# Performance work log

Measured on AMD Instinct MI355X. Metric: run time of the kernel, lower is better.

## Reference

```python
import jax, jax.numpy as jnp
import numpy as np

EMBD = 768
FFN_HID = 2048
HEAD_DIM = 64
KV_H = 5
KV_DIM = KV_H * HEAD_DIM
Q_H = 15
EPS = 1.1920929e-07  # torch.finfo(float32).eps, nn.RMSNorm default when eps=None
MAX_WAVELENGTH = 10000.0


def rmsnorm(x, w):
    var = jnp.mean(x * x, axis=-1, keepdims=True)
    return x * jax.lax.rsqrt(var + EPS) * w


def apply_rope(q, L):
    # q: [B, L, H, D]; rotate-half RoPE applied only to queries (as in source)
    d_half = HEAD_DIM // 2
    ts = MAX_WAVELENGTH ** (2.0 / HEAD_DIM * jnp.arange(d_half, dtype=jnp.float32))
    pos = jnp.arange(L, dtype=jnp.float32)
    radians = pos[:, None] / ts[None, :]            # [L, d_half]
    s = jnp.sin(radians)[None, :, None, :]          # [1, L, 1, d_half]
    c = jnp.cos(radians)[None, :, None, :]
    q1, q2 = q[..., :d_half], q[..., d_half:]
    return jnp.concatenate([q1 * c - q2 * s, q2 * c + q1 * s], axis=-1)


def setup_inputs() -> dict:
    key = jax.random.key(0)
    ks = jax.random.split(key, 12)
    B, L, Lc = 4, 512, 2048
    sc = 0.02
    return {
        "x": jax.random.normal(ks[0], (B, L, EMBD), jnp.float32),
        "text_k": jax.random.normal(ks[1], (B, Lc, KV_DIM), jnp.float32),
        "text_v": jax.random.normal(ks[2], (B, Lc, KV_DIM), jnp.float32),
        "ln1_w": jnp.ones((EMBD,), jnp.float32),
        "ln2_w": jnp.ones((EMBD,), jnp.float32),
        "wq": jax.random.normal(ks[3], (EMBD, Q_H * HEAD_DIM), jnp.float32) * sc,
        "wk": jax.random.normal(ks[4], (KV_DIM, KV_DIM), jnp.float32) * sc,
        "wv": jax.random.normal(ks[5], (KV_DIM, KV_DIM), jnp.float32) * sc,
        "wo": jax.random.normal(ks[6], (Q_H * HEAD_DIM, EMBD), jnp.float32) * sc,
        "w_gate": jax.random.normal(ks[7], (EMBD, FFN_HID), jnp.float32) * sc,
        "w_up": jax.random.normal(ks[8], (EMBD, FFN_HID), jnp.float32) * sc,
        "w_down": jax.random.normal(ks[9], (FFN_HID, EMBD), jnp.float32) * sc,
    }


def reference(x, text_k, text_v, ln1_w, ln2_w, wq, wk, wv, wo, w_gate, w_up, w_down):
    B, L, _ = x.shape
    Lc = text_k.shape[1]

    residual = x
    x_norm = rmsnorm(x, ln1_w)
    q = (x_norm @ wq).reshape(B, L, Q_H, HEAD_DIM)
    k = (text_k @ wk).reshape(B, Lc, KV_H, HEAD_DIM)
    v = (text_v @ wv).reshape(B, Lc, KV_H, HEAD_DIM)

    q = apply_rope(q, L)

    # GQA: each of the 15 query heads maps to one of 5 kv heads
    kv_map = (jnp.arange(Q_H) * KV_H) // Q_H        # [0,0,0,1,1,1,...,4,4,4]
    k_sel = k[:, :, kv_map, :]                       # [B, Lc, Q_H, D]
    v_sel = v[:, :, kv_map, :]

    scores = jnp.einsum("blhd,bmhd->bhlm", q, k_sel) / (HEAD_DIM ** 0.5)
    attn = jax.nn.softmax(scores, axis=-1)
    ctx = jnp.einsum("bhlm,bmhd->blhd", attn, v_sel).reshape(B, L, Q_H * HEAD_DIM)

    x = ctx @ wo + residual

    residual = x
    xn = rmsnorm(x, ln2_w)
    h = jax.nn.silu(xn @ w_gate) * (xn @ w_up)       # SwiGLU
    return h @ w_down + residual
```

## Files before the change

### kernel.cpp

```cpp
#include <hip/hip_runtime.h>
#include <hip/hip_bf16.h>
#include <math.h>

#define EMBD 768
#define FFN_HID 2048
#define HEAD_DIM 64
#define KV_H 5
#define KV_DIM 320
#define Q_H 15
#define QDIM (Q_H * HEAD_DIM)
#define BB 4
#define LL 512
#define LC 2048
#define EPSV 1.1920929e-07f

typedef __attribute__((ext_vector_type(8))) __bf16 bf16x8;
typedef __attribute__((ext_vector_type(2))) __bf16 bf16x2;
typedef __attribute__((ext_vector_type(8))) short short8;
typedef __attribute__((ext_vector_type(4))) float floatx4;
typedef __attribute__((ext_vector_type(2))) unsigned uint2v;
typedef unsigned short ushort;

#define RSCALE 0.18033688011112042f

__device__ inline ushort f2bf(float f) {
  union { float f; unsigned u; } c; c.f = f;
  return (ushort)((c.u + 0x8000u) >> 16);
}
__device__ inline float bf2f(ushort s) {
  union { unsigned u; float f; } c; c.u = ((unsigned)s) << 16;
  return c.f;
}
#if __has_builtin(__builtin_amdgcn_cvt_pk_bf16_f32)
__device__ inline unsigned pk2bf(float a, float b) {
  union { bf16x2 v; unsigned u; } c;
  c.v = __builtin_amdgcn_cvt_pk_bf16_f32(a, b);
  return c.u;
}
#else
__device__ inline unsigned pk2bf(float a, float b) {
  union { float f; unsigned u; } x, y; x.f = a; y.f = b;
  return ((x.u + 0x8000u) >> 16) | ((y.u + 0x8000u) & 0xffff0000u);
}
#endif

__device__ __forceinline__ void glds16(const ushort* g, ushort* l) {
  __builtin_amdgcn_global_load_lds(
      (const __attribute__((address_space(1))) unsigned int*)g,
      (__attribute__((address_space(3))) unsigned int*)l, 16, 0, 0);
}

__global__ __launch_bounds__(256) void rmsnorm_kernel(const float* __restrict__ x,
                                                      const float* __restrict__ w,
                                                      ushort* __restrict__ out) {
  int row = blockIdx.x;
  const float* xr = x + (size_t)row * EMBD;
  ushort* orow = out + (size_t)row * EMBD;
  int tid = threadIdx.x;
  float ss = 0.f;
  for (int i = tid; i < EMBD; i += 256) { float v = xr[i]; ss += v * v; }
  for (int off = 32; off > 0; off >>= 1) ss += __shfl_down(ss, off, 64);
  __shared__ float sred[4];
  if ((tid & 63) == 0) sred[tid >> 6] = ss;
  __syncthreads();
  float tot = sred[0] + sred[1] + sred[2] + sred[3];
  float scale = rsqrtf(tot * (1.0f / EMBD) + EPSV);
  for (int i = tid; i < EMBD; i += 256) orow[i] = f2bf(xr[i] * scale * w[i]);
}

struct MD { const void* src; void* dst; const float* aux; int K; int N; int nx; int base; int mode; };
struct MD10 { MD d[10]; };

__global__ __launch_bounds__(256) void mega_prep(MD10 ds) {
  int bid = blockIdx.x;
  int sel = 0;
#pragma unroll
  for (int j = 1; j < 10; ++j) sel = (bid >= ds.d[j].base) ? j : sel;
  MD t = ds.d[sel];
  int rel = bid - t.base;
  int tid = threadIdx.x;
  if (t.mode == 1) {
    int i = rel * 256 + tid;
    float4 f = *(const float4*)((const float*)t.src + (size_t)i * 4);
    ushort* o = (ushort*)t.dst + (size_t)i * 4;
    o[0] = f2bf(f.x); o[1] = f2bf(f.y); o[2] = f2bf(f.z); o[3] = f2bf(f.w);
    return;
  }
  if (t.mode == 2) {
    const float* xr = (const float*)t.src + (size_t)rel * EMBD;
    ushort* orow = (ushort*)t.dst + (size_t)rel * EMBD;
    float ss = 0.f;
    for (int i = tid; i < EMBD; i += 256) { float v = xr[i]; ss += v * v; }
    for (int off = 32; off > 0; off >>= 1) ss += __shfl_down(ss, off, 64);
    __shared__ float sred[4];
    if ((tid & 63) == 0) sred[tid >> 6] = ss;
    __syncthreads();
    float tot = sred[0] + sred[1] + sred[2] + sred[3];
    float scale = rsqrtf(tot * (1.0f / EMBD) + EPSV);
    for (int i = tid; i < EMBD; i += 256) orow[i] = f2bf(xr[i] * scale * t.aux[i]);
    return;
  }
  int bx = rel % t.nx, by = rel / t.nx;
  int k0 = by * 64, n0 = bx * 64;
  __shared__ ushort T[64][72];
  int r = tid >> 2, cb = (tid & 3) * 16;
#pragma unroll
  for (int i = 0; i < 16; i += 4) {
    float4 f = *(const float4*)((const float*)t.src + (size_t)(k0 + r) * t.N + n0 + cb + i);
    T[r][cb + i + 0] = f2bf(f.x); T[r][cb + i + 1] = f2bf(f.y);
    T[r][cb + i + 2] = f2bf(f.z); T[r][cb + i + 3] = f2bf(f.w);
  }
  __syncthreads();
#pragma unroll
  for (int i = 0; i < 2; ++i) {
    short8 v;
#pragma unroll
    for (int j = 0; j < 8; ++j) v[j] = (short)T[cb + i * 8 + j][r];
    *(short8*)((ushort*)t.dst + (size_t)(n0 + r) * t.K + k0 + cb + i * 8) = v;
  }
}

template <int OM>
__global__ __launch_bounds__(256) void gemm64(const ushort* __restrict__ A,
                                              const ushort* __restrict__ Bt,
                                              const float* __restrict__ Rf,
                                              void* __restrict__ Cout,
                                              int M, int N, int K) {
  __shared__ ushort As[64 * 64];
  __shared__ ushort Bs[64 * 64];
  int tid = threadIdx.x;
  int w = tid >> 6, lane = tid & 63;
  int lm = lane & 15, lq = lane >> 4;
  int m0 = blockIdx.y * 64, n0 = blockIdx.x * 64;
  int wm = (w & 1) * 32, wn = (w >> 1) * 32;
  int arow = lane >> 3, acol = ((lane & 7) ^ arow) << 3;
  int kg[2] = {((lq) ^ (lm & 7)) << 3, ((4 + lq) ^ (lm & 7)) << 3};
  floatx4 acc[2][2];
#pragma unroll
  for (int i = 0; i < 2; ++i)
#pragma unroll
    for (int j = 0; j < 2; ++j) acc[i][j] = (floatx4){0.f, 0.f, 0.f, 0.f};
  for (int k0 = 0; k0 < K; k0 += 64) {
#pragma unroll
    for (int s = 0; s < 2; ++s) {
      int g = (w << 1) + s;
      glds16(A + (size_t)(m0 + g * 8 + arow) * K + k0 + acol, &As[g * 512]);
      glds16(Bt + (size_t)(n0 + g * 8 + arow) * K + k0 + acol, &Bs[g * 512]);
    }
    __syncthreads();
#pragma unroll
    for (int kc = 0; kc < 2; ++kc) {
      bf16x8 af[2], bf[2];
#pragma unroll
      for (int mt = 0; mt < 2; ++mt)
        af[mt] = *(const bf16x8*)&As[(wm + mt * 16 + lm) * 64 + kg[kc]];
#pragma unroll
      for (int nt = 0; nt < 2; ++nt)
        bf[nt] = *(const bf16x8*)&Bs[(wn + nt * 16 + lm) * 64 + kg[kc]];
#pragma unroll
      for (int mt = 0; mt < 2; ++mt)
#pragma unroll
        for (int nt = 0; nt < 2; ++nt)
          acc[mt][nt] = __builtin_amdgcn_mfma_f32_16x16x32_bf16(af[mt], bf[nt], acc[mt][nt], 0, 0, 0);
    }
    __syncthreads();
  }
#pragma unroll
  for (int mt = 0; mt < 2; ++mt)
#pragma unroll
    for (int nt = 0; nt < 2; ++nt)
#pragma unroll
      for (int r = 0; r < 4; ++r) {
        int row = m0 + wm + mt * 16 + lq * 4 + r;
        int col = n0 + wn + nt * 16 + lm;
        size_t idx = (size_t)row * N + col;
        float vv = acc[mt][nt][r];
        if (OM == 1) ((float*)Cout)[idx] = vv + Rf[idx];
        if (OM == 2) ((ushort*)Cout)[idx] = f2bf(vv);
      }
}

__global__ __launch_bounds__(256) void gemm_kv128(const ushort* __restrict__ Ak,
                                                  const ushort* __restrict__ Av,
                                                  const ushort* __restrict__ Btk,
                                                  const ushort* __restrict__ Btv,
                                                  ushort* __restrict__ Ck,
                                                  ushort* __restrict__ Vt,
                                                  int M, int N, int K) {
  const ushort* A = blockIdx.z ? Av : Ak;
  const ushort* Bt = blockIdx.z ? Btv : Btk;
  __shared__ ushort As[128 * 64];
  __shared__ ushort Bs[64 * 64];
  int tid = threadIdx.x;
  int w = tid >> 6, lane = tid & 63;
  int lm = lane & 15, lq = lane >> 4;
  int m0 = blockIdx.y * 128, n0 = blockIdx.x * 64;
  int wm = (w & 1) * 64, wn = (w >> 1) * 32;
  int arow = lane >> 3, acol = ((lane & 7) ^ arow) << 3;
  int kg[2] = {((lq) ^ (lm & 7)) << 3, ((4 + lq) ^ (lm & 7)) << 3};
  floatx4 acc[4][2];
#pragma unroll
  for (int i = 0; i < 4; ++i)
#pragma unroll
    for (int j = 0; j < 2; ++j) acc[i][j] = (floatx4){0.f, 0.f, 0.f, 0.f};
  for (int k0 = 0; k0 < K; k0 += 64) {
#pragma unroll
    for (int s = 0; s < 4; ++s) {
      int g = (w << 2) + s;
      glds16(A + (size_t)(m0 + g * 8 + arow) * K + k0 + acol, &As[g * 512]);
    }
#pragma unroll
    for (int s = 0; s < 2; ++s) {
      int g = (w << 1) + s;
      glds16(Bt + (size_t)(n0 + g * 8 + arow) * K + k0 + acol, &Bs[g * 512]);
    }
    __syncthreads();
#pragma unroll
    for (int kc = 0; kc < 2; ++kc) {
      bf16x8 af[4], bf[2];
#pragma unroll
      for (int mt = 0; mt < 4; ++mt)
        af[mt] = *(const bf16x8*)&As[(wm + mt * 16 + lm) * 64 + kg[kc]];
#pragma unroll
      for (int nt = 0; nt < 2; ++nt)
        bf[nt] = *(const bf16x8*)&Bs[(wn + nt * 16 + lm) * 64 + kg[kc]];
#pragma unroll
      for (int mt = 0; mt < 4; ++mt)
#pragma unroll
        for (int nt = 0; nt < 2; ++nt)
          acc[mt][nt] = __builtin_amdgcn_mfma_f32_16x16x32_bf16(af[mt], bf[nt], acc[mt][nt], 0, 0, 0);
    }
    __syncthreads();
  }
  if (blockIdx.z == 0) {
#pragma unroll
    for (int mt = 0; mt < 4; ++mt)
#pragma unroll
      for (int nt = 0; nt < 2; ++nt)
#pragma unroll
        for (int r = 0; r < 4; ++r) {
          int row = m0 + wm + mt * 16 + lq * 4 + r;
          int col = n0 + wn + nt * 16 + lm;
          Ck[(size_t)row * N + col] = f2bf(acc[mt][nt][r]);
        }
  } else {
    int kvh = n0 >> 6;
#pragma unroll
    for (int mt = 0; mt < 4; ++mt)
#pragma unroll
      for (int nt = 0; nt < 2; ++nt) {
        int d = wn + nt * 16 + lm;
        int grow = m0 + wm + mt * 16 + lq * 4;
        int b = grow >> 11;
        int tok = grow & (LC - 1);
        size_t a = ((size_t)(b * KV_H + kvh) * 64 + d) * LC + tok;
        uint2v pk = (uint2v){pk2bf(acc[mt][nt][0], acc[mt][nt][1]),
                             pk2bf(acc[mt][nt][2], acc[mt][nt][3])};
        *(uint2v*)&Vt[a] = pk;
      }
  }
}

__global__ __launch_bounds__(256) void gemm_q_rope(const ushort* __restrict__ A,
                                                   const ushort* __restrict__ Bt,
                                                   ushort* __restrict__ Q,
                                                   int M, int N, int K) {
  __shared__ ushort As[128 * 64];
  __shared__ ushort Bs[64 * 64];
  int tid = threadIdx.x;
  int w = tid >> 6, lane = tid & 63;
  int lm = lane & 15, lq = lane >> 4;
  int m0 = blockIdx.y * 128, n0 = blockIdx.x * 64;
  int wm = (w & 1) * 64, wn = (w >> 1) * 16;
  int arow = lane >> 3, acol = ((lane & 7) ^ arow) << 3;
  int kg[2] = {((lq) ^ (lm & 7)) << 3, ((4 + lq) ^ (lm & 7)) << 3};
  floatx4 acc[4][2];
#pragma unroll
  for (int i = 0; i < 4; ++i)
#pragma unroll
    for (int j = 0; j < 2; ++j) acc[i][j] = (floatx4){0.f, 0.f, 0.f, 0.f};
  for (int k0 = 0; k0 < K; k0 += 64) {
#pragma unroll
    for (int s = 0; s < 4; ++s) {
      int g = (w << 2) + s;
      glds16(A + (size_t)(m0 + g * 8 + arow) * K + k0 + acol, &As[g * 512]);
    }
#pragma unroll
    for (int s = 0; s < 2; ++s) {
      int g = (w << 1) + s;
      glds16(Bt + (size_t)(n0 + g * 8 + arow) * K + k0 + acol, &Bs[g * 512]);
    }
    __syncthreads();
#pragma unroll
    for (int kc = 0; kc < 2; ++kc) {
      bf16x8 af[4], bf[2];
#pragma unroll
      for (int mt = 0; mt < 4; ++mt)
        af[mt] = *(const bf16x8*)&As[(wm + mt * 16 + lm) * 64 + kg[kc]];
#pragma unroll
      for (int nt = 0; nt < 2; ++nt) {
        int br = wn + nt * 32 + lm;
        bf[nt] = *(const bf16x8*)&Bs[br * 64 + (((kc * 4 + lq) ^ (br & 7)) << 3)];
      }
#pragma unroll
      for (int mt = 0; mt < 4; ++mt)
#pragma unroll
        for (int nt = 0; nt < 2; ++nt)
          acc[mt][nt] = __builtin_amdgcn_mfma_f32_16x16x32_bf16(af[mt], bf[nt], acc[mt][nt], 0, 0, 0);
    }
    __syncthreads();
  }
  int d = wn + lm;
  float invts = exp2f(-(float)d * 0.4152410118609203f);
#pragma unroll
  for (int mt = 0; mt < 4; ++mt)
#pragma unroll
    for (int r = 0; r < 4; ++r) {
      int row = m0 + wm + mt * 16 + lq * 4 + r;
      int l = row & (LL - 1);
      float th = (float)l * invts;
      float s, c;
      __sincosf(th, &s, &c);
      float q1 = acc[mt][0][r], q2 = acc[mt][1][r];
      size_t base = (size_t)row * N + n0 + d;
      Q[base] = f2bf((q1 * c - q2 * s) * RSCALE);
      Q[base + 32] = f2bf((q2 * c + q1 * s) * RSCALE);
    }
}

__global__ __launch_bounds__(256) void gemm_gateup(const ushort* __restrict__ A,
                                                   const ushort* __restrict__ Bg,
                                                   const ushort* __restrict__ Bu,
                                                   ushort* __restrict__ H,
                                                   int M, int N, int K) {
  __shared__ ushort As[128 * 64];
  __shared__ ushort Bs0[64 * 64];
  __shared__ ushort Bs1[64 * 64];
  int tid = threadIdx.x;
  int w = tid >> 6, lane = tid & 63;
  int lm = lane & 15, lq = lane >> 4;
  int m0 = blockIdx.y * 128, n0 = blockIdx.x * 64;
  int wm = (w & 1) * 64, wn = (w >> 1) * 32;
  int arow = lane >> 3, acol = ((lane & 7) ^ arow) << 3;
  int kg[2] = {((lq) ^ (lm & 7)) << 3, ((4 + lq) ^ (lm & 7)) << 3};
  floatx4 accg[4][2], accu[4][2];
#pragma unroll
  for (int i = 0; i < 4; ++i)
#pragma unroll
    for (int j = 0; j < 2; ++j) {
      accg[i][j] = (floatx4){0.f, 0.f, 0.f, 0.f};
      accu[i][j] = (floatx4){0.f, 0.f, 0.f, 0.f};
    }
  for (int k0 = 0; k0 < K; k0 += 64) {
#pragma unroll
    for (int s = 0; s < 4; ++s) {
      int g = (w << 2) + s;
      glds16(A + (size_t)(m0 + g * 8 + arow) * K + k0 + acol, &As[g * 512]);
    }
#pragma unroll
    for (int s = 0; s < 2; ++s) {
      int g = (w << 1) + s;
      glds16(Bg + (size_t)(n0 + g * 8 + arow) * K + k0 + acol, &Bs0[g * 512]);
      glds16(Bu + (size_t)(n0 + g * 8 + arow) * K + k0 + acol, &Bs1[g * 512]);
    }
    __syncthreads();
#pragma unroll
    for (int kc = 0; kc < 2; ++kc) {
      bf16x8 af[4], bg[2], bu[2];
#pragma unroll
      for (int mt = 0; mt < 4; ++mt)
        af[mt] = *(const bf16x8*)&As[(wm + mt * 16 + lm) * 64 + kg[kc]];
#pragma unroll
      for (int nt = 0; nt < 2; ++nt) {
        bg[nt] = *(const bf16x8*)&Bs0[(wn + nt * 16 + lm) * 64 + kg[kc]];
        bu[nt] = *(const bf16x8*)&Bs1[(wn + nt * 16 + lm) * 64 + kg[kc]];
      }
#pragma unroll
      for (int mt = 0; mt < 4; ++mt)
#pragma unroll
        for (int nt = 0; nt < 2; ++nt) {
          accg[mt][nt] = __builtin_amdgcn_mfma_f32_16x16x32_bf16(af[mt], bg[nt], accg[mt][nt], 0, 0, 0);
          accu[mt][nt] = __builtin_amdgcn_mfma_f32_16x16x32_bf16(af[mt], bu[nt], accu[mt][nt], 0, 0, 0);
        }
    }
    __syncthreads();
  }
#pragma unroll
  for (int mt = 0; mt < 4; ++mt)
#pragma unroll
    for (int nt = 0; nt < 2; ++nt)
#pragma unroll
      for (int r = 0; r < 4; ++r) {
        int row = m0 + wm + mt * 16 + lq * 4 + r;
        int col = n0 + wn + nt * 16 + lm;
        float gv = accg[mt][nt][r];
        float hv = gv / (1.f + __expf(-gv)) * accu[mt][nt][r];
        H[(size_t)row * N + col] = f2bf(hv);
      }
}

__global__ __launch_bounds__(256) void attn_kernel(const ushort* __restrict__ qb,
                                                   const ushort* __restrict__ kb,
                                                   const ushort* __restrict__ vt,
                                                   ushort* __restrict__ Op,
                                                   float* __restrict__ Ml) {
  int bid = blockIdx.x;
  int g = bid / 48, wi = bid - g * 48;
  int b = g / 5, kvh = g - b * 5;
  int hsub = wi % 3;
  int t2 = wi / 3;
  int lt = t2 & 7, sp = t2 >> 3;
  int h = kvh * 3 + hsub;
  int l0 = lt * 64;
  int kv0 = sp * 1024;
  __shared__ ushort Qs[64 * 64];
  __shared__ ushort Ks[64 * 64];
  __shared__ ushort Vs[64 * 64];
  __shared__ ushort Ps[4][16][72];
  int tid = threadIdx.x;
  int w = tid >> 6, lane = tid & 63, lm = lane & 15, lq = lane >> 4;
  int arow = lane >> 3, acol = ((lane & 7) ^ arow) << 3;
  int kg[2] = {((lq) ^ (lm & 7)) << 3, ((4 + lq) ^ (lm & 7)) << 3};
#pragma unroll
  for (int s = 0; s < 2; ++s) {
    int gg = (w << 1) + s;
    glds16(qb + (size_t)(b * LL + l0 + gg * 8 + arow) * QDIM + h * HEAD_DIM + acol, &Qs[gg * 512]);
  }
  __syncthreads();
  bf16x8 aq[2];
  {
    int qr = w * 16 + lm;
    aq[0] = *(const bf16x8*)&Qs[qr * 64 + (((lq) ^ (qr & 7)) << 3)];
    aq[1] = *(const bf16x8*)&Qs[qr * 64 + (((4 + lq) ^ (qr & 7)) << 3)];
  }
  bf16x8 bones;
  {
    short8 o = {0x3F80, 0x3F80, 0x3F80, 0x3F80, 0x3F80, 0x3F80, 0x3F80, 0x3F80};
    bones = *(bf16x8*)&o;
  }
  floatx4 oacc[4];
#pragma unroll
  for (int i = 0; i < 4; ++i) oacc[i] = (floatx4){0.f, 0.f, 0.f, 0.f};
  floatx4 lacc = (floatx4){0.f, 0.f, 0.f, 0.f};

  for (int m0 = kv0; m0 < kv0 + 1024; m0 += 64) {
#pragma unroll
    for (int s = 0; s < 2; ++s) {
      int gg = (w << 1) + s;
      glds16(kb + (size_t)(b * LC + m0 + gg * 8 + arow) * KV_DIM + kvh * HEAD_DIM + acol, &Ks[gg * 512]);
      glds16(vt + ((size_t)(b * KV_H + kvh) * 64 + gg * 8 + arow) * LC + m0 + acol, &Vs[gg * 512]);
    }
    __syncthreads();

    floatx4 sacc[4];
#pragma unroll
    for (int nt = 0; nt < 4; ++nt) sacc[nt] = (floatx4){0.f, 0.f, 0.f, 0.f};
#pragma unroll
    for (int kc = 0; kc < 2; ++kc) {
#pragma unroll
      for (int nt = 0; nt < 4; ++nt) {
        bf16x8 bk = *(const bf16x8*)&Ks[(nt * 16 + lm) * 64 + kg[kc]];
        sacc[nt] = __builtin_amdgcn_mfma_f32_16x16x32_bf16(bk, aq[kc], sacc[nt], 0, 0, 0);
      }
    }
#pragma unroll
    for (int nt = 0; nt < 4; ++nt) {
      float p0 = exp2f(sacc[nt][0]);
      float p1 = exp2f(sacc[nt][1]);
      float p2 = exp2f(sacc[nt][2]);
      float p3 = exp2f(sacc[nt][3]);
      uint2v pk = (uint2v){pk2bf(p0, p1), pk2bf(p2, p3)};
      *(uint2v*)&Ps[w][lm][nt * 16 + lq * 4] = pk;
    }
#pragma unroll
    for (int kc2 = 0; kc2 < 2; ++kc2) {
      bf16x8 ap = *(const bf16x8*)&Ps[w][lm][kc2 * 32 + lq * 8];
#pragma unroll
      for (int dt = 0; dt < 4; ++dt) {
        bf16x8 bv = *(const bf16x8*)&Vs[(dt * 16 + lm) * 64 + kg[kc2]];
        oacc[dt] = __builtin_amdgcn_mfma_f32_16x16x32_bf16(ap, bv, oacc[dt], 0, 0, 0);
      }
      lacc = __builtin_amdgcn_mfma_f32_16x16x32_bf16(ap, bones, lacc, 0, 0, 0);
    }
    __syncthreads();
  }
#pragma unroll
  for (int r = 0; r < 4; ++r) {
    int row = l0 + w * 16 + lq * 4 + r;
    size_t base = ((size_t)sp * (BB * LL) + b * LL + row) * QDIM + h * HEAD_DIM;
#pragma unroll
    for (int dt = 0; dt < 4; ++dt) Op[base + dt * 16 + lm] = f2bf(oacc[dt][r]);
    if (lm == 0) Ml[((size_t)sp * (BB * LL) + b * LL + row) * Q_H + h] = lacc[r];
  }
}

__global__ __launch_bounds__(256) void combine_kernel(ushort* __restrict__ Op,
                                                      const float* __restrict__ Ml,
                                                      ushort* __restrict__ ctx) {
  int bl = blockIdx.x, t = threadIdx.x;
  if (t >= 240) return;
  int h = t >> 4, d4 = (t & 15) * 4;
  float la = Ml[(size_t)bl * Q_H + h];
  float lb = Ml[((size_t)(BB * LL) + bl) * Q_H + h];
  float inv = 1.f / (la + lb);
  size_t i0 = (size_t)bl * QDIM + h * HEAD_DIM + d4;
  size_t i1 = (size_t)(BB * LL) * QDIM + i0;
#pragma unroll
  for (int j = 0; j < 4; ++j) {
    float o = (bf2f(Op[i0 + j]) + bf2f(Op[i1 + j])) * inv;
    ctx[i0 + j] = f2bf(o);
  }
}

extern "C" void kernel_launch(void* const* d_in, const int* in_sizes, int n_in,
                              void* d_out, int out_size, void* d_ws, size_t ws_size,
                              hipStream_t stream) {
  const float* x      = (const float*)d_in[0];
  const float* text_k = (const float*)d_in[1];
  const float* text_v = (const float*)d_in[2];
  const float* ln1_w  = (const float*)d_in[3];
  const float* ln2_w  = (const float*)d_in[4];
  const float* wq     = (const float*)d_in[5];
  const float* wk     = (const float*)d_in[6];
  const float* wv     = (const float*)d_in[7];
  const float* wo     = (const float*)d_in[8];
  const float* w_gate = (const float*)d_in[9];
  const float* w_up   = (const float*)d_in[10];
  const float* w_down = (const float*)d_in[11];
  float* out = (float*)d_out;
  char* base = (char*)d_ws;

  const int BL = BB * LL;
  const int BLC = BB * LC;

  ushort* xnorm = (ushort*)(base + 0);
  ushort* wqt   = (ushort*)(base + 3145728);
  ushort* wkt   = (ushort*)(base + 4620288);
  ushort* wvt   = (ushort*)(base + 4825088);
  ushort* wot   = (ushort*)(base + 5029888);
  ushort* wgt   = (ushort*)(base + 6504448);
  ushort* wut   = (ushort*)(base + 9650176);
  ushort* wdt   = (ushort*)(base + 12795904);
  ushort* kbuf  = (ushort*)(base + 15941632);
  ushort* vtb   = (ushort*)(base + 21184512);
  float*  x2    = (float*) (base + 26427392);
  ushort* qb    = (ushort*)(base + 32718848);
  float*  Ml    = (float*) (base + 36651008);
  ushort* tkb   = (ushort*)(base + 37142528);
  ushort* tvb   = (ushort*)(base + 42385408);
  char* SCR = base + 47628288;
  ushort* Op    = (ushort*)SCR;
  ushort* ctxb  = (ushort*)SCR;
  ushort* gbuf  = (ushort*)(base + 15941632);

  MD10 ds;
  const int NKV4 = BLC * KV_DIM / 1024;
  ds.d[0] = {wq,     wqt,   nullptr, EMBD,    QDIM,    QDIM / 64,    0,    0};
  ds.d[1] = {wk,     wkt,   nullptr, KV_DIM,  KV_DIM,  KV_DIM / 64,  180,  0};
  ds.d[2] = {wv,     wvt,   nullptr, KV_DIM,  KV_DIM,  KV_DIM / 64,  205,  0};
  ds.d[3] = {wo,     wot,   nullptr, QDIM,    EMBD,    EMBD / 64,    230,  0};
  ds.d[4] = {w_gate, wgt,   nullptr, EMBD,    FFN_HID, FFN_HID / 64, 410,  0};
  ds.d[5] = {w_up,   wut,   nullptr, EMBD,    FFN_HID, FFN_HID / 64, 794,  0};
  ds.d[6] = {w_down, wdt,   nullptr, FFN_HID, EMBD,    EMBD / 64,    1178, 0};
  ds.d[7] = {text_k, tkb,   nullptr, 0, 0, 0, 1562, 1};
  ds.d[8] = {text_v, tvb,   nullptr, 0, 0, 0, 1562 + NKV4, 1};
  ds.d[9] = {x,      xnorm, ln1_w,   0, 0, 0, 1562 + 2 * NKV4, 2};
  const int nmega = 1562 + 2 * NKV4 + BL;
  mega_prep<<<nmega, 256, 0, stream>>>(ds);

  gemm_kv128<<<dim3(KV_DIM / 64, BLC / 128, 2), 256, 0, stream>>>(tkb, tvb, wkt, wvt, kbuf, vtb, BLC, KV_DIM, KV_DIM);

  gemm_q_rope<<<dim3(QDIM / 64, BL / 128), 256, 0, stream>>>(xnorm, wqt, qb, BL, QDIM, EMBD);

  attn_kernel<<<960, 256, 0, stream>>>(qb, kbuf, vtb, Op, Ml);
  combine_kernel<<<BL, 256, 0, stream>>>(Op, Ml, ctxb);

  gemm64<1><<<dim3(EMBD / 64, BL / 64), 256, 0, stream>>>(ctxb, wot, x, x2, BL, EMBD, QDIM);

  rmsnorm_kernel<<<BL, 256, 0, stream>>>(x2, ln2_w, xnorm);
  gemm_gateup<<<dim3(FFN_HID / 64, BL / 128), 256, 0, stream>>>(xnorm, wgt, wut, gbuf, BL, FFN_HID, EMBD);
  gemm64<1><<<dim3(EMBD / 64, BL / 64), 256, 0, stream>>>(gbuf, wdt, x2, out, BL, EMBD, FFN_HID);
}
```

Baseline: 144.3 us.

## Widen attention query tile to 128 rows and split KV four ways

Each attention block now processes 128 query rows (32 per wave) against a 512-key slice instead of 64 rows against 1024 keys. Every K/V tile loaded into shared memory therefore feeds twice as many MFMAs, and the Q staging buffer reuses the P scratch space. The KV range is split into four partitions instead of two, so the combine kernel sums four partial outputs and denominators. The cost is more per-wave registers and extra partial-output traffic, and the launch code must provide workspace for four splits.

Result: no change. 146.6 us (+1.6%).

```diff
diff --git a/kernel.cpp b/kernel.cpp
--- a/kernel.cpp
+++ b/kernel.cpp
@@ -13,6 +13,7 @@
 #define LL 512
 #define LC 2048
 #define EPSV 1.1920929e-07f
+#define NSP 4
 
 typedef __attribute__((ext_vector_type(8))) __bf16 bf16x8;
 typedef __attribute__((ext_vector_type(2))) __bf16 bf16x2;
@@ -405,45 +406,48 @@
                                                    ushort* __restrict__ Op,
                                                    float* __restrict__ Ml) {
   int bid = blockIdx.x;
-  int g = bid / 48, wi = bid - g * 48;
-  int b = g / 5, kvh = g - b * 5;
-  int hsub = wi % 3;
-  int t2 = wi / 3;
-  int lt = t2 & 7, sp = t2 >> 3;
-  int h = kvh * 3 + hsub;
-  int l0 = lt * 64;
-  int kv0 = sp * 1024;
-  __shared__ ushort Qs[64 * 64];
+  int sp = bid & 3;
+  int qt = (bid >> 2) & 3;
+  int g = bid >> 4;
+  int b = g / 15, h = g - b * 15;
+  int kvh = h / 3;
+  int l0 = qt * 128;
+  int kv0 = sp * 512;
   __shared__ ushort Ks[64 * 64];
   __shared__ ushort Vs[64 * 64];
-  __shared__ ushort Ps[4][16][72];
+  __shared__ ushort Ps[4][32][72];
+  ushort* Qs = &Ps[0][0][0];
   int tid = threadIdx.x;
   int w = tid >> 6, lane = tid & 63, lm = lane & 15, lq = lane >> 4;
   int arow = lane >> 3, acol = ((lane & 7) ^ arow) << 3;
   int kg[2] = {((lq) ^ (lm & 7)) << 3, ((4 + lq) ^ (lm & 7)) << 3};
 #pragma unroll
-  for (int s = 0; s < 2; ++s) {
-    int gg = (w << 1) + s;
+  for (int s = 0; s < 4; ++s) {
+    int gg = (w << 2) + s;
     glds16(qb + (size_t)(b * LL + l0 + gg * 8 + arow) * QDIM + h * HEAD_DIM + acol, &Qs[gg * 512]);
   }
   __syncthreads();
-  bf16x8 aq[2];
-  {
-    int qr = w * 16 + lm;
-    aq[0] = *(const bf16x8*)&Qs[qr * 64 + (((lq) ^ (qr & 7)) << 3)];
-    aq[1] = *(const bf16x8*)&Qs[qr * 64 + (((4 + lq) ^ (qr & 7)) << 3)];
+  bf16x8 aq[2][2];
+#pragma unroll
+  for (int q2 = 0; q2 < 2; ++q2) {
+    int qr = w * 32 + q2 * 16 + lm;
+    aq[q2][0] = *(const bf16x8*)&Qs[qr * 64 + kg[0]];
+    aq[q2][1] = *(const bf16x8*)&Qs[qr * 64 + kg[1]];
   }
   bf16x8 bones;
   {
     short8 o = {0x3F80, 0x3F80, 0x3F80, 0x3F80, 0x3F80, 0x3F80, 0x3F80, 0x3F80};
     bones = *(bf16x8*)&o;
   }
-  floatx4 oacc[4];
-#pragma unroll
-  for (int i = 0; i < 4; ++i) oacc[i] = (floatx4){0.f, 0.f, 0.f, 0.f};
-  floatx4 lacc = (floatx4){0.f, 0.f, 0.f, 0.f};
-
-  for (int m0 = kv0; m0 < kv0 + 1024; m0 += 64) {
+  floatx4 oacc[4][2];
+#pragma unroll
+  for (int i = 0; i < 4; ++i)
+#pragma unroll
+    for (int j = 0; j < 2; ++j) oacc[i][j] = (floatx4){0.f, 0.f, 0.f, 0.f};
+  floatx4 lacc[2] = {(floatx4){0.f, 0.f, 0.f, 0.f}, (floatx4){0.f, 0.f, 0.f, 0.f}};
+
+  for (int t = 0; t < 8; ++t) {
+    int m0 = kv0 + t * 64;
 #pragma unroll
     for (int s = 0; s < 2; ++s) {
       int gg = (w << 1) + s;
@@ -452,46 +456,59 @@
     }
     __syncthreads();
 
-    floatx4 sacc[4];
-#pragma unroll
-    for (int nt = 0; nt < 4; ++nt) sacc[nt] = (floatx4){0.f, 0.f, 0.f, 0.f};
+    floatx4 sacc[4][2];
+#pragma unroll
+    for (int nt = 0; nt < 4; ++nt)
+#pragma unroll
+      for (int q2 = 0; q2 < 2; ++q2) sacc[nt][q2] = (floatx4){0.f, 0.f, 0.f, 0.f};
 #pragma unroll
     for (int kc = 0; kc < 2; ++kc) {
 #pragma unroll
       for (int nt = 0; nt < 4; ++nt) {
         bf16x8 bk = *(const bf16x8*)&Ks[(nt * 16 + lm) * 64 + kg[kc]];
-        sacc[nt] = __builtin_amdgcn_mfma_f32_16x16x32_bf16(bk, aq[kc], sacc[nt], 0, 0, 0);
-      }
-    }
-#pragma unroll
-    for (int nt = 0; nt < 4; ++nt) {
-      float p0 = exp2f(sacc[nt][0]);
-      float p1 = exp2f(sacc[nt][1]);
-      float p2 = exp2f(sacc[nt][2]);
-      float p3 = exp2f(sacc[nt][3]);
-      uint2v pk = (uint2v){pk2bf(p0, p1), pk2bf(p2, p3)};
-      *(uint2v*)&Ps[w][lm][nt * 16 + lq * 4] = pk;
-    }
+#pragma unroll
+        for (int q2 = 0; q2 < 2; ++q2)
+          sacc[nt][q2] = __builtin_amdgcn_mfma_f32_16x16x32_bf16(bk, aq[q2][kc], sacc[nt][q2], 0, 0, 0);
+      }
+    }
+#pragma unroll
+    for (int nt = 0; nt < 4; ++nt)
+#pragma unroll
+      for (int q2 = 0; q2 < 2; ++q2) {
+        float p0 = exp2f(sacc[nt][q2][0]);
+        float p1 = exp2f(sacc[nt][q2][1]);
+        float p2 = exp2f(sacc[nt][q2][2]);
+        float p3 = exp2f(sacc[nt][q2][3]);
+        uint2v pk = (uint2v){pk2bf(p0, p1), pk2bf(p2, p3)};
+        *(uint2v*)&Ps[w][q2 * 16 + lm][nt * 16 + lq * 4] = pk;
+      }
 #pragma unroll
     for (int kc2 = 0; kc2 < 2; ++kc2) {
-      bf16x8 ap = *(const bf16x8*)&Ps[w][lm][kc2 * 32 + lq * 8];
+      bf16x8 ap[2];
+      ap[0] = *(const bf16x8*)&Ps[w][lm][kc2 * 32 + lq * 8];
+      ap[1] = *(const bf16x8*)&Ps[w][16 + lm][kc2 * 32 + lq * 8];
 #pragma unroll
       for (int dt = 0; dt < 4; ++dt) {
         bf16x8 bv = *(const bf16x8*)&Vs[(dt * 16 + lm) * 64 + kg[kc2]];
-        oacc[dt] = __builtin_amdgcn_mfma_f32_16x16x32_bf16(ap, bv, oacc[dt], 0, 0, 0);
-      }
-      lacc = __builtin_amdgcn_mfma_f32_16x16x32_bf16(ap, bones, lacc, 0, 0, 0);
-    }
-    __syncthreads();
-  }
-#pragma unroll
-  for (int r = 0; r < 4; ++r) {
-    int row = l0 + w * 16 + lq * 4 + r;
-    size_t base = ((size_t)sp * (BB * LL) + b * LL + row) * QDIM + h * HEAD_DIM;
-#pragma unroll
-    for (int dt = 0; dt < 4; ++dt) Op[base + dt * 16 + lm] = f2bf(oacc[dt][r]);
-    if (lm == 0) Ml[((size_t)sp * (BB * LL) + b * LL + row) * Q_H + h] = lacc[r];
-  }
+#pragma unroll
+        for (int q2 = 0; q2 < 2; ++q2)
+          oacc[dt][q2] = __builtin_amdgcn_mfma_f32_16x16x32_bf16(ap[q2], bv, oacc[dt][q2], 0, 0, 0);
+      }
+      lacc[0] = __builtin_amdgcn_mfma_f32_16x16x32_bf16(ap[0], bones, lacc[0], 0, 0, 0);
+      lacc[1] = __builtin_amdgcn_mfma_f32_16x16x32_bf16(ap[1], bones, lacc[1], 0, 0, 0);
+    }
+    __syncthreads();
+  }
+#pragma unroll
+  for (int q2 = 0; q2 < 2; ++q2)
+#pragma unroll
+    for (int r = 0; r < 4; ++r) {
+      int row = l0 + w * 32 + q2 * 16 + lq * 4 + r;
+      size_t base = ((size_t)sp * (BB * LL) + b * LL + row) * QDIM + h * HEAD_DIM;
+#pragma unroll
+      for (int dt = 0; dt < 4; ++dt) Op[base + dt * 16 + lm] = f2bf(oacc[dt][q2][r]);
+      if (lm == 0) Ml[((size_t)sp * (BB * LL) + b * LL + row) * Q_H + h] = lacc[q2][r];
+    }
 }
 
 __global__ __launch_bounds__(256) void combine_kernel(ushort* __restrict__ Op,
@@ -500,16 +517,20 @@
   int bl = blockIdx.x, t = threadIdx.x;
   if (t >= 240) return;
   int h = t >> 4, d4 = (t & 15) * 4;
-  float la = Ml[(size_t)bl * Q_H + h];
-  float lb = Ml[((size_t)(BB * LL) + bl) * Q_H + h];
-  float inv = 1.f / (la + lb);
+  float lsum = 0.f;
+#pragma unroll
+  for (int s = 0; s < NSP; ++s) lsum += Ml[((size_t)s * (BB * LL) + bl) * Q_H + h];
+  float inv = 1.f / lsum;
   size_t i0 = (size_t)bl * QDIM + h * HEAD_DIM + d4;
-  size_t i1 = (size_t)(BB * LL) * QDIM + i0;
-#pragma unroll
-  for (int j = 0; j < 4; ++j) {
-    float o = (bf2f(Op[i0 + j]) + bf2f(Op[i1 + j])) * inv;
-    ctx[i0 + j] = f2bf(o);
-  }
+  float o[4] = {0.f, 0.f, 0.f, 0.f};
+#pragma unroll
+  for (int s = 0; s < NSP; ++s) {
+    const ushort* p = Op + (size_t)s * (BB * LL) * QDIM + i0;
+#pragma unroll
+    for (int j = 0; j < 4; ++j) o[j] += bf2f(p[j]);
+  }
+#pragma unroll
+  for (int j = 0; j < 4; ++j) ctx[i0 + j] = f2bf(o[j] * inv);
 }
 
 extern "C" void kernel_launch(void* const* d_in, const int* in_sizes, int n_in,
```
